# Kernel optimization log

Measured on AMD Instinct MI355X. Metric: run time of the kernel, lower is better.

The kernel has to match this reference:

```python
import jax, jax.numpy as jnp
import numpy as np
import math

D_MODEL = 1024
HIDDEN = 1024
NUM_HEADS = 16
D_K = D_MODEL // NUM_HEADS  # 64
B, S = 4, 2048


def setup_inputs() -> dict:
    key = jax.random.key(0)
    ks = jax.random.split(key, 11)
    sc_in = 1.0 / math.sqrt(D_MODEL)
    sc_h = 1.0 / math.sqrt(HIDDEN)
    return {
        "k": jax.random.normal(ks[0], (B, S, D_MODEL), jnp.float32),
        "q": jax.random.normal(ks[1], (B, S, D_MODEL), jnp.float32),
        "v": jax.random.normal(ks[2], (B, S, D_MODEL), jnp.float32),
        "Wq": jax.random.normal(ks[3], (HIDDEN, D_MODEL), jnp.float32) * sc_in,
        "bq": jnp.zeros((HIDDEN,), jnp.float32),
        "Wk": jax.random.normal(ks[4], (HIDDEN, D_MODEL), jnp.float32) * sc_in,
        "bk": jnp.zeros((HIDDEN,), jnp.float32),
        "Wv": jax.random.normal(ks[5], (HIDDEN, D_MODEL), jnp.float32) * sc_in,
        "bv": jnp.zeros((HIDDEN,), jnp.float32),
        "Wo": jax.random.normal(ks[6], (HIDDEN, HIDDEN), jnp.float32) * sc_h,
        "bo": jnp.zeros((HIDDEN,), jnp.float32),
    }


def _split_heads(x):
    # [B, S, HIDDEN] -> [B, H, S, d_k]
    b, s, _ = x.shape
    return x.reshape(b, s, NUM_HEADS, D_K).transpose(0, 2, 1, 3)


def reference(k, q, v, Wq, bq, Wk, bk, Wv, bv, Wo, bo):
    qp = _split_heads(q @ Wq.T + bq)
    kp = _split_heads(k @ Wk.T + bk)
    vp = _split_heads(v @ Wv.T + bv)
    inv_sqrt_dk = 1.0 / math.sqrt(D_K)
    # [B, H, Sq, Sk]
    mult = jnp.einsum("bhqd,bhkd->bhqk", qp, kp) * inv_sqrt_dk
    # torch f.softmax without dim on a 4D tensor -> dim=1 (heads axis)
    w = jax.nn.softmax(mult, axis=1)
    w = jax.nn.softmax(w * inv_sqrt_dk, axis=1)  # second softmax, same implicit dim
    val = jnp.einsum("bhqk,bhkd->bhqd", w, vp)
    val = val.transpose(0, 2, 1, 3).reshape(q.shape[0], q.shape[1], HIDDEN)
    return val @ Wo.T + bo
```

## Files before the change

### kernel.cpp

```cpp
#include <hip/hip_runtime.h>
#include <math.h>

#define BB 4
#define SS 2048
#define DM 1024
#define NH 16

typedef unsigned short u16;
typedef __attribute__((ext_vector_type(8))) short bf16x8;
typedef __attribute__((ext_vector_type(4))) float f32x4;

__device__ __forceinline__ u16 f2bf(float f) {
  union { float f; unsigned u; } v; v.f = f;
  unsigned r = v.u + 0x7fffu + ((v.u >> 16) & 1u);
  return (u16)(r >> 16);
}
__device__ __forceinline__ float bf2f(u16 h) {
  union { unsigned u; float f; } v; v.u = ((unsigned)h) << 16;
  return v.f;
}
__device__ __forceinline__ void gl16(const u16* g, u16* l) {
  __builtin_amdgcn_global_load_lds((__attribute__((address_space(1))) void*)(u16*)g,
                                   (__attribute__((address_space(3))) void*)l, 16, 0, 0);
}

#define BARRIER_LDS()                                    \
  do {                                                   \
    __builtin_amdgcn_sched_barrier(0);                   \
    asm volatile("s_waitcnt lgkmcnt(0)" ::: "memory");   \
    __builtin_amdgcn_s_barrier();                        \
    __builtin_amdgcn_sched_barrier(0);                   \
  } while (0)

__global__ __launch_bounds__(256) void cvt_bf16(const float* __restrict__ in,
                                                u16* __restrict__ out, int n8) {
  int i = blockIdx.x * 256 + threadIdx.x;
  if (i >= n8) return;
  const float4* p = (const float4*)in + (size_t)i * 2;
  float4 a = p[0], b = p[1];
  ushort4 o0 = { f2bf(a.x), f2bf(a.y), f2bf(a.z), f2bf(a.w) };
  ushort4 o1 = { f2bf(b.x), f2bf(b.y), f2bf(b.z), f2bf(b.w) };
  ushort4* q = (ushort4*)out + (size_t)i * 2;
  q[0] = o0; q[1] = o1;
}

template <int MODE>
__global__ __launch_bounds__(256) void gemm_proj(const u16* __restrict__ A,
                                                 const u16* __restrict__ W,
                                                 const float* __restrict__ bias,
                                                 void* __restrict__ Cv,
                                                 int M, int N, int K) {
  __shared__ __align__(16) u16 As[128 * 32];
  __shared__ __align__(16) u16 Bs[128 * 32];
  const int t = threadIdx.x;
  const int w = t >> 6, l = t & 63;
  const int m0 = blockIdx.x * 128, n0 = blockIdx.y * 128;
  const int wm = (w >> 1) * 64, wn = (w & 1) * 64;
  const int lr = l & 15, lg = (l >> 4) * 8;
  const int sr = t >> 2, sc4 = (t & 3) * 8;

  const u16* Ap1 = A + (size_t)(m0 + sr) * K + sc4;
  const u16* Ap2 = Ap1 + (size_t)64 * K;
  const u16* Wp1 = W + (size_t)(n0 + sr) * K + sc4;
  const u16* Wp2 = Wp1 + (size_t)64 * K;
  u16* Asd1 = As + w * 512;
  u16* Asd2 = As + 2048 + w * 512;
  u16* Bsd1 = Bs + w * 512;
  u16* Bsd2 = Bs + 2048 + w * 512;

  f32x4 acc[4][4];
  f32x4 z4 = {0.f, 0.f, 0.f, 0.f};
#pragma unroll
  for (int i = 0; i < 4; ++i)
#pragma unroll
    for (int j = 0; j < 4; ++j) acc[i][j] = z4;

  for (int k0 = 0; k0 < K; k0 += 32) {
    __syncthreads();
    gl16(Ap1 + k0, Asd1);
    gl16(Ap2 + k0, Asd2);
    gl16(Wp1 + k0, Bsd1);
    gl16(Wp2 + k0, Bsd2);
    __syncthreads();
    bf16x8 af[4], bw[4];
#pragma unroll
    for (int i = 0; i < 4; ++i) {
      af[i] = *(const bf16x8*)&As[(wm + i * 16 + lr) * 32 + lg];
      bw[i] = *(const bf16x8*)&Bs[(wn + i * 16 + lr) * 32 + lg];
    }
#pragma unroll
    for (int i = 0; i < 4; ++i)
#pragma unroll
      for (int j = 0; j < 4; ++j)
        acc[i][j] = __builtin_amdgcn_mfma_f32_16x16x32_bf16(af[i], bw[j], acc[i][j], 0, 0, 0);
  }

  const int lg4 = (l >> 4) * 4;
#pragma unroll
  for (int j = 0; j < 4; ++j) {
    const int col = n0 + wn + j * 16 + lr;
    const float bj = bias[col];
#pragma unroll
    for (int i = 0; i < 4; ++i) {
#pragma unroll
      for (int r = 0; r < 4; ++r) {
        const int row = m0 + wm + i * 16 + lg4 + r;
        const float val = acc[i][j][r] + bj;
        if (MODE == 0) {
          ((u16*)Cv)[(size_t)row * N + col] = f2bf(val);
        } else if (MODE == 1) {
          ((u16*)Cv)[((size_t)((row >> 11) * 16 + (col >> 6)) * 64 + (col & 63)) * SS +
                     (row & 2047)] = f2bf(val);
        } else {
          ((float*)Cv)[(size_t)row * N + col] = val;
        }
      }
    }
  }
}

__device__ __forceinline__ void dsm16(float x[16]) {
  float m = x[0];
#pragma unroll
  for (int h = 1; h < 16; ++h) m = fmaxf(m, x[h]);
  float s = 0.f;
#pragma unroll
  for (int h = 0; h < 16; ++h) { x[h] = __expf(x[h] - m); s += x[h]; }
  const float inv = 0.125f / s;
  float s2 = 0.f;
#pragma unroll
  for (int h = 0; h < 16; ++h) { x[h] = __expf((x[h] - 1.0f) * inv); s2 += x[h]; }
  const float inv2 = 1.f / s2;
#pragma unroll
  for (int h = 0; h < 16; ++h) x[h] *= inv2;
}

#define WROW 40
#define WPLANE (32 * WROW)
__global__ __launch_bounds__(512, 2) void fused_attn(const u16* __restrict__ Qp,
                                                     const u16* __restrict__ Kp,
                                                     const u16* __restrict__ Vt,
                                                     u16* __restrict__ AO) {
  __shared__ __align__(16) u16 Ws[2][16 * WPLANE];

  const int t = threadIdx.x;
  const int w = t >> 6, l = t & 63;
  const int lr = l & 15, lg = l >> 4;
  const int bid = blockIdx.x;
  const int xcd = bid & 7;
  const int b = xcd >> 1;
  const int qt = (xcd & 1) * 32 + (bid >> 3);
  const int q0 = qt * 32;
  const int h0 = w * 2;

  bf16x8 qf[2][2][2];
#pragma unroll
  for (int hh = 0; hh < 2; ++hh)
#pragma unroll
    for (int m = 0; m < 2; ++m)
#pragma unroll
      for (int dc = 0; dc < 2; ++dc)
        qf[hh][m][dc] = *(const bf16x8*)(Qp + ((size_t)b * SS + q0 + m * 16 + lr) * DM +
                                         (h0 + hh) * 64 + dc * 32 + lg * 8);

  const u16* kb = Kp + ((size_t)b * SS + lr) * DM + h0 * 64 + lg * 8;
  const u16* vb = Vt + (((size_t)b * 16 + h0) * 64 + lr) * SS + lg * 8;

  f32x4 o[2][2][4];
  f32x4 z4 = {0.f, 0.f, 0.f, 0.f};
#pragma unroll
  for (int hh = 0; hh < 2; ++hh)
#pragma unroll
    for (int m = 0; m < 2; ++m)
#pragma unroll
      for (int d = 0; d < 4; ++d) o[hh][m][d] = z4;

  const int sq = t >> 4;
  const int sk = t & 15;

  bf16x8 kfr[8], vfr[8];
#pragma unroll
  for (int hh = 0; hh < 2; ++hh)
#pragma unroll
    for (int dc = 0; dc < 2; ++dc)
#pragma unroll
      for (int n = 0; n < 2; ++n)
        kfr[hh * 4 + dc * 2 + n] =
            *(const bf16x8*)(kb + (size_t)(n * 16) * DM + hh * 64 + dc * 32);
#pragma unroll
  for (int hh = 0; hh < 2; ++hh)
#pragma unroll
    for (int ds = 0; ds < 4; ++ds)
      vfr[hh * 4 + ds] = *(const bf16x8*)(vb + (size_t)(hh * 64 + ds * 16) * SS);

  for (int tt = 0; tt < 64; ++tt) {
    u16* Wsb = &Ws[tt & 1][0];
    const size_t knext = (size_t)(((tt + 1) & 63) * 32) * DM;
    const int vnext = ((tt + 1) & 63) * 32;

    f32x4 sa[2][2][2];
#pragma unroll
    for (int hh = 0; hh < 2; ++hh)
#pragma unroll
      for (int n = 0; n < 2; ++n)
#pragma unroll
        for (int m = 0; m < 2; ++m) sa[hh][n][m] = z4;
#pragma unroll
    for (int hh = 0; hh < 2; ++hh)
#pragma unroll
      for (int dc = 0; dc < 2; ++dc)
#pragma unroll
        for (int n = 0; n < 2; ++n)
#pragma unroll
          for (int m = 0; m < 2; ++m)
            sa[hh][n][m] = __builtin_amdgcn_mfma_f32_16x16x32_bf16(
                kfr[hh * 4 + dc * 2 + n], qf[hh][m][dc], sa[hh][n][m], 0, 0, 0);
#pragma unroll
    for (int hh = 0; hh < 2; ++hh)
#pragma unroll
      for (int n = 0; n < 2; ++n)
#pragma unroll
        for (int m = 0; m < 2; ++m) {
          ushort4 pk = { f2bf(sa[hh][n][m][0] * 0.125f), f2bf(sa[hh][n][m][1] * 0.125f),
                         f2bf(sa[hh][n][m][2] * 0.125f), f2bf(sa[hh][n][m][3] * 0.125f) };
          *(ushort4*)&Wsb[(h0 + hh) * WPLANE + (m * 16 + lr) * WROW + n * 16 + lg * 4] = pk;
        }
#pragma unroll
    for (int hh = 0; hh < 2; ++hh)
#pragma unroll
      for (int dc = 0; dc < 2; ++dc)
#pragma unroll
        for (int n = 0; n < 2; ++n)
          kfr[hh * 4 + dc * 2 + n] =
              *(const bf16x8*)(kb + knext + (size_t)(n * 16) * DM + hh * 64 + dc * 32);
    BARRIER_LDS();

    {
      u16* fib = Wsb + sq * WROW + sk * 2;
      float xa[16], xb[16];
#pragma unroll
      for (int h = 0; h < 16; ++h) {
        const unsigned u = *(const unsigned*)(fib + h * WPLANE);
        xa[h] = bf2f((u16)(u & 0xffffu));
        xb[h] = bf2f((u16)(u >> 16));
      }
      dsm16(xa);
      dsm16(xb);
#pragma unroll
      for (int h = 0; h < 16; ++h)
        *(unsigned*)(fib + h * WPLANE) = (unsigned)f2bf(xa[h]) | ((unsigned)f2bf(xb[h]) << 16);
    }
    BARRIER_LDS();

#pragma unroll
    for (int hh = 0; hh < 2; ++hh) {
      bf16x8 aw[2];
#pragma unroll
      for (int m = 0; m < 2; ++m)
        aw[m] = *(const bf16x8*)&Wsb[(h0 + hh) * WPLANE + (m * 16 + lr) * WROW + lg * 8];
#pragma unroll
      for (int ds = 0; ds < 4; ++ds)
#pragma unroll
        for (int m = 0; m < 2; ++m)
          o[hh][m][ds] = __builtin_amdgcn_mfma_f32_16x16x32_bf16(aw[m], vfr[hh * 4 + ds],
                                                                 o[hh][m][ds], 0, 0, 0);
    }
#pragma unroll
    for (int hh = 0; hh < 2; ++hh)
#pragma unroll
      for (int ds = 0; ds < 4; ++ds)
        vfr[hh * 4 + ds] = *(const bf16x8*)(vb + vnext + (size_t)(hh * 64 + ds * 16) * SS);
  }

#pragma unroll
  for (int hh = 0; hh < 2; ++hh)
#pragma unroll
    for (int m = 0; m < 2; ++m)
#pragma unroll
      for (int ds = 0; ds < 4; ++ds)
#pragma unroll
        for (int r = 0; r < 4; ++r)
          AO[((size_t)b * SS + q0 + m * 16 + lg * 4 + r) * DM + (h0 + hh) * 64 + ds * 16 + lr] =
              f2bf(o[hh][m][ds][r]);
}

extern "C" void kernel_launch(void* const* d_in, const int* in_sizes, int n_in,
                              void* d_out, int out_size, void* d_ws, size_t ws_size,
                              hipStream_t stream) {
  const float* kin = (const float*)d_in[0];
  const float* qin = (const float*)d_in[1];
  const float* vin = (const float*)d_in[2];
  const float* Wq  = (const float*)d_in[3];
  const float* bq  = (const float*)d_in[4];
  const float* Wk  = (const float*)d_in[5];
  const float* bk  = (const float*)d_in[6];
  const float* Wv  = (const float*)d_in[7];
  const float* bv  = (const float*)d_in[8];
  const float* Wo  = (const float*)d_in[9];
  const float* bo  = (const float*)d_in[10];

  const size_t P   = (size_t)BB * SS * DM;
  const size_t WSZ = (size_t)DM * DM;
  u16* Qb  = (u16*)d_ws;
  u16* Kb  = Qb + P;
  u16* Vb  = Kb + P;
  u16* Wqb = Vb + P;
  u16* Wkb = Wqb + WSZ;
  u16* Wvb = Wkb + WSZ;
  u16* Wob = Wvb + WSZ;
  u16* Qp  = Wob + WSZ;
  u16* Kp  = Qp + P;
  u16* Vt  = Kp + P;
  u16* AO  = Vt + P;

  cvt_bf16<<<dim3(4096), 256, 0, stream>>>(qin, Qb, (int)(P / 8));
  cvt_bf16<<<dim3(4096), 256, 0, stream>>>(kin, Kb, (int)(P / 8));
  cvt_bf16<<<dim3(4096), 256, 0, stream>>>(vin, Vb, (int)(P / 8));
  cvt_bf16<<<dim3(512), 256, 0, stream>>>(Wq, Wqb, (int)(WSZ / 8));
  cvt_bf16<<<dim3(512), 256, 0, stream>>>(Wk, Wkb, (int)(WSZ / 8));
  cvt_bf16<<<dim3(512), 256, 0, stream>>>(Wv, Wvb, (int)(WSZ / 8));
  cvt_bf16<<<dim3(512), 256, 0, stream>>>(Wo, Wob, (int)(WSZ / 8));

  dim3 gp(64, 8);
  gemm_proj<0><<<gp, 256, 0, stream>>>(Qb, Wqb, bq, Qp, 8192, 1024, 1024);
  gemm_proj<0><<<gp, 256, 0, stream>>>(Kb, Wkb, bk, Kp, 8192, 1024, 1024);
  gemm_proj<1><<<gp, 256, 0, stream>>>(Vb, Wvb, bv, Vt, 8192, 1024, 1024);

  fused_attn<<<dim3(256), 512, 0, stream>>>(Qp, Kp, Vt, AO);

  gemm_proj<2><<<gp, 256, 0, stream>>>(AO, Wob, bo, (float*)d_out, 8192, 1024, 1024);
}
```

Before: 627.0 us.

## Split attention over key halves and combine fp32 partial outputs

The softmax here runs over heads, not keys, so each key's weight is independent and the attention output sums cleanly over keys. The attention kernel now splits the key range in two, launching twice as many blocks. Each block writes an fp32 partial output, and a new combine kernel adds the two partials and converts the result to bf16. This is meant to fix underuse of the GPU, where the old grid gave roughly one block per CU. In exchange it adds extra fp32 global-memory traffic and one more launch, and the raised launch-bounds occupancy hint may tighten the register budget and cause spills.

```diff
diff --git a/kernel.cpp b/kernel.cpp
--- a/kernel.cpp
+++ b/kernel.cpp
@@ -42,6 +42,17 @@
   ushort4 o1 = { f2bf(b.x), f2bf(b.y), f2bf(b.z), f2bf(b.w) };
   ushort4* q = (ushort4*)out + (size_t)i * 2;
   q[0] = o0; q[1] = o1;
+}
+
+__global__ __launch_bounds__(256) void combine_o(const float* __restrict__ p0,
+                                                 const float* __restrict__ p1,
+                                                 u16* __restrict__ out, int n4) {
+  int i = blockIdx.x * 256 + threadIdx.x;
+  if (i >= n4) return;
+  float4 a = ((const float4*)p0)[i];
+  float4 b = ((const float4*)p1)[i];
+  ushort4 o = { f2bf(a.x + b.x), f2bf(a.y + b.y), f2bf(a.z + b.z), f2bf(a.w + b.w) };
+  ((ushort4*)out)[i] = o;
 }
 
 template <int MODE>
@@ -137,10 +148,10 @@
 
 #define WROW 40
 #define WPLANE (32 * WROW)
-__global__ __launch_bounds__(512, 2) void fused_attn(const u16* __restrict__ Qp,
+__global__ __launch_bounds__(512, 4) void fused_attn(const u16* __restrict__ Qp,
                                                      const u16* __restrict__ Kp,
                                                      const u16* __restrict__ Vt,
-                                                     u16* __restrict__ AO) {
+                                                     float* __restrict__ pO) {
   __shared__ __align__(16) u16 Ws[2][16 * WPLANE];
 
   const int t = threadIdx.x;
@@ -149,9 +160,12 @@
   const int bid = blockIdx.x;
   const int xcd = bid & 7;
   const int b = xcd >> 1;
-  const int qt = (xcd & 1) * 32 + (bid >> 3);
+  const int kh = xcd & 1;
+  const int qt = bid >> 3;
   const int q0 = qt * 32;
+  const int ks0 = kh * (SS / 2);
   const int h0 = w * 2;
+  const size_t P = (size_t)BB * SS * DM;
 
   bf16x8 qf[2][2][2];
 #pragma unroll
@@ -163,8 +177,9 @@
         qf[hh][m][dc] = *(const bf16x8*)(Qp + ((size_t)b * SS + q0 + m * 16 + lr) * DM +
                                          (h0 + hh) * 64 + dc * 32 + lg * 8);
 
-  const u16* kb = Kp + ((size_t)b * SS + lr) * DM + h0 * 64 + lg * 8;
-  const u16* vb = Vt + (((size_t)b * 16 + h0) * 64 + lr) * SS + lg * 8;
+  const u16* kb = Kp + ((size_t)b * SS + ks0 + lr) * DM + h0 * 64 + lg * 8;
+  const u16* vb = Vt + (((size_t)b * 16 + h0) * 64 + lr) * SS + ks0 + lg * 8;
+  float* po = pO + (size_t)kh * P;
 
   f32x4 o[2][2][4];
   f32x4 z4 = {0.f, 0.f, 0.f, 0.f};
@@ -193,10 +208,10 @@
     for (int ds = 0; ds < 4; ++ds)
       vfr[hh * 4 + ds] = *(const bf16x8*)(vb + (size_t)(hh * 64 + ds * 16) * SS);
 
-  for (int tt = 0; tt < 64; ++tt) {
+  for (int tt = 0; tt < 32; ++tt) {
     u16* Wsb = &Ws[tt & 1][0];
-    const size_t knext = (size_t)(((tt + 1) & 63) * 32) * DM;
-    const int vnext = ((tt + 1) & 63) * 32;
+    const size_t knext = (size_t)(((tt + 1) & 31) * 32) * DM;
+    const int vnext = ((tt + 1) & 31) * 32;
 
     f32x4 sa[2][2][2];
 #pragma unroll
@@ -280,8 +295,8 @@
       for (int ds = 0; ds < 4; ++ds)
 #pragma unroll
         for (int r = 0; r < 4; ++r)
-          AO[((size_t)b * SS + q0 + m * 16 + lg * 4 + r) * DM + (h0 + hh) * 64 + ds * 16 + lr] =
-              f2bf(o[hh][m][ds][r]);
+          po[((size_t)b * SS + q0 + m * 16 + lg * 4 + r) * DM + (h0 + hh) * 64 + ds * 16 + lr] =
+              o[hh][m][ds][r];
 }
 
 extern "C" void kernel_launch(void* const* d_in, const int* in_sizes, int n_in,
@@ -312,6 +327,7 @@
   u16* Kp  = Qp + P;
   u16* Vt  = Kp + P;
   u16* AO  = Vt + P;
+  float* pO = (float*)(AO + P);
 
   cvt_bf16<<<dim3(4096), 256, 0, stream>>>(qin, Qb, (int)(P / 8));
   cvt_bf16<<<dim3(4096), 256, 0, stream>>>(kin, Kb, (int)(P / 8));
@@ -326,7 +342,9 @@
   gemm_proj<0><<<gp, 256, 0, stream>>>(Kb, Wkb, bk, Kp, 8192, 1024, 1024);
   gemm_proj<1><<<gp, 256, 0, stream>>>(Vb, Wvb, bv, Vt, 8192, 1024, 1024);
 
-  fused_attn<<<dim3(256), 512, 0, stream>>>(Qp, Kp, Vt, AO);
+  fused_attn<<<dim3(512), 512, 0, stream>>>(Qp, Kp, Vt, pO);
+
+  combine_o<<<dim3((int)(P / 4 / 256)), 256, 0, stream>>>(pO, pO + P, AO, (int)(P / 4));
 
   gemm_proj<2><<<gp, 256, 0, stream>>>(AO, Wob, bo, (float*)d_out, 8192, 1024, 1024);
 }
```

Measured after the change: 1.046 ms. 1.67x slower.
